# Optimization experiments

Measured on AMD Instinct MI355X. Metric: run time of the kernel, lower is better.

Reference implementation:

```python
import jax, jax.numpy as jnp
import numpy as np

B, N, D_IN = 8192, 32, 128   # batch, num_agents, obs_input_dim
D_PROC = 128                 # obs_output_dim
D_FIN = 128                  # final_input_dim
HID = 256                    # hard-coded policy hidden
A = 10                       # final_output_dim (num_actions)


def setup_inputs() -> dict:
    key = jax.random.key(0)
    ks = jax.random.split(key, 9)
    s = lambda k, shp: jax.random.normal(k, shp, dtype=jnp.float32) / jnp.sqrt(jnp.float32(shp[-1]))
    return {
        "states": jax.random.normal(ks[0], (B, N, D_IN), dtype=jnp.float32),
        "Wk1": s(ks[1], (D_PROC, D_IN)),
        "Wq1": s(ks[2], (D_PROC, D_IN)),
        "Wv1": s(ks[3], (D_PROC, D_IN)),
        "Wk2": s(ks[4], (D_FIN, D_PROC)),
        "Wq2": s(ks[5], (D_FIN, D_PROC)),
        "Wv2": s(ks[6], (D_FIN, D_PROC)),
        "Wp1": s(ks[7], (HID, D_FIN)),
        "Wp2": s(ks[8], (A, HID)),
    }


def reference(states, Wk1, Wq1, Wv1, Wk2, Wq2, Wv2, Wp1, Wp2):
    # NOTE: the original torch code scales BOTH attention blocks by
    # sqrt(self.d_k_obs) == sqrt(final_input_dim) (not d_k_obs_proc).
    inv_scale = 1.0 / jnp.sqrt(jnp.asarray(Wk2.shape[0], states.dtype))

    # ---- attention block 1 over agents ----
    k1 = jnp.einsum("bnd,ed->bne", states, Wk1)
    q1 = jnp.einsum("bnd,ed->bne", states, Wq1)
    v1 = jnp.einsum("bnd,ed->bne", states, Wv1)
    weight_1 = jax.nn.softmax(jnp.einsum("bne,bme->bnm", q1, k1) * inv_scale, axis=-1)
    wav = jnp.einsum("bnm,bme->bne", weight_1, v1)  # [B, N, D_PROC]

    # ---- attention block 2 ----
    k2 = jnp.einsum("bne,fe->bnf", wav, Wk2)
    q2 = jnp.einsum("bne,fe->bnf", wav, Wq2)
    v2 = jnp.einsum("bne,fe->bnf", wav, Wv2)
    weight = jax.nn.softmax(jnp.einsum("bnf,bmf->bnm", q2, k2) * inv_scale, axis=-1)
    node_features = jnp.einsum("bnm,bmf->bnf", weight, v2)  # [B, N, D_FIN]

    # ---- policy MLP head ----
    h = jax.nn.leaky_relu(jnp.einsum("bnf,hf->bnh", node_features, Wp1), negative_slope=0.01)
    policy = jax.nn.softmax(jnp.einsum("bnh,ah->bna", h, Wp2), axis=-1)
    return policy, weight_1, weight
```

## Files before the change

kernel.cpp:

```cpp
#include <hip/hip_runtime.h>
#include <stdint.h>

namespace {

typedef __attribute__((ext_vector_type(8)))  short short8;
typedef __attribute__((ext_vector_type(16))) float f32x16;
typedef __attribute__((ext_vector_type(4)))  float f32x4;

union U4 {
    uint4    q;
    uint32_t u[4];
    uint16_t us[8];
    short8   s8;
};

constexpr float INV_SCALE = 0.08838834764831845f;

constexpr size_t WSPROJ  = 32768;
constexpr size_t WP1OFF  = 4 * WSPROJ;
constexpr size_t WP2OFF  = WP1OFF + 65536;
constexpr size_t M1F_OFF = WP2OFF + 16384;
constexpr size_t M2F_OFF = M1F_OFF + 65536;

constexpr int AH_OFF = 0;
constexpr int TB_OFF = 16384;
constexpr int VT_OFF = 32768;
constexpr int S_OFF  = 49152;

__device__ __forceinline__ int pl_addr(int base, int n, int e) {
    return base + ((n * 256 + e * 2) ^ ((n & 15) << 4));
}
__device__ __forceinline__ int vt_addr(int e, int m) {
    return VT_OFF + ((e * 128 + m * 2) ^ ((e & 7) << 4));
}
__device__ __forceinline__ int s_addr(int n, int m) {
    return S_OFF + n * 144 + m * 4;
}
__device__ __forceinline__ int h_addr(int n, int h) {
    return TB_OFF + ((n * 512 + h * 2) ^ ((n & 15) << 4));
}
__device__ __forceinline__ int ps_addr(int n, int a) {
    return AH_OFF + n * 144 + a * 4;
}

__device__ __forceinline__ uint16_t f2bf_rne(float x) {
    uint32_t u = __float_as_uint(x);
    u += 0x7FFFu + ((u >> 16) & 1u);
    return (uint16_t)(u >> 16);
}

__device__ __forceinline__ uint32_t pack2_rne(float x0, float x1) {
    uint32_t u0 = __float_as_uint(x0); u0 += 0x7FFFu + ((u0 >> 16) & 1u);
    uint32_t u1 = __float_as_uint(x1); u1 += 0x7FFFu + ((u1 >> 16) & 1u);
    return __builtin_amdgcn_perm(u1, u0, 0x07060302u);
}

__device__ __forceinline__ void split8(float4 a, float4 b, short8& hi, short8& lo) {
    float xs[8] = {a.x, a.y, a.z, a.w, b.x, b.y, b.z, b.w};
    U4 h, l;
#pragma unroll
    for (int p = 0; p < 4; ++p) {
        uint32_t b0 = __float_as_uint(xs[2 * p]);
        uint32_t b1 = __float_as_uint(xs[2 * p + 1]);
        float r0 = xs[2 * p]     - __uint_as_float(b0 & 0xFFFF0000u);
        float r1 = xs[2 * p + 1] - __uint_as_float(b1 & 0xFFFF0000u);
        h.u[p] = __builtin_amdgcn_perm(b1, b0, 0x07060302u);
        l.u[p] = __builtin_amdgcn_perm(__float_as_uint(r1), __float_as_uint(r0), 0x07060302u);
    }
    hi = h.s8; lo = l.s8;
}

__device__ __forceinline__ void gemm_tv(const char* smem, const uint8_t* __restrict__ wb,
                                        int rowoff, int c, int l,
                                        f32x16& tacc, f32x16& vacc) {
    f32x16 z = {0.f,0.f,0.f,0.f, 0.f,0.f,0.f,0.f, 0.f,0.f,0.f,0.f, 0.f,0.f,0.f,0.f};
    tacc = z; vacc = z;
    const int n = rowoff + (l & 31), half = l >> 5;
#pragma unroll 1
    for (int kb = 0; kb < 8; ++kb) {
        const int d0 = kb * 16 + half * 8;
        U4 ah;
        ah.q = *(const uint4*)(smem + pl_addr(AH_OFF, n, d0));
        const uint8_t* p = wb + (size_t)(c * 8 + kb) * 1024 + (size_t)l * 16;
        U4 bm, bv;
        bm.q = *(const uint4*)p;
        tacc = __builtin_amdgcn_mfma_f32_32x32x16_bf16(ah.s8, bm.s8, tacc, 0, 0, 0);
        bv.q = *(const uint4*)(p + WSPROJ);
        vacc = __builtin_amdgcn_mfma_f32_32x32x16_bf16(ah.s8, bv.s8, vacc, 0, 0, 0);
    }
}

__device__ __forceinline__ void gemm_mlp2(const char* smem, const uint8_t* __restrict__ mb,
                                          int rowoff, int c, int l,
                                          f32x16& a0, f32x16& a1) {
    f32x16 z = {0.f,0.f,0.f,0.f, 0.f,0.f,0.f,0.f, 0.f,0.f,0.f,0.f, 0.f,0.f,0.f,0.f};
    a0 = z; a1 = z;
    const int n = rowoff + (l & 31), half = l >> 5;
#pragma unroll 1
    for (int kb = 0; kb < 8; ++kb) {
        const int d0 = kb * 16 + half * 8;
        U4 ah;
        ah.q = *(const uint4*)(smem + pl_addr(AH_OFF, n, d0));
        const uint8_t* p0 = mb + (size_t)((c)     * 8 + kb) * 1024 + (size_t)l * 16;
        const uint8_t* p1 = mb + (size_t)((c + 4) * 8 + kb) * 1024 + (size_t)l * 16;
        U4 b0, b1;
        b0.q = *(const uint4*)p0;
        a0 = __builtin_amdgcn_mfma_f32_32x32x16_bf16(ah.s8, b0.s8, a0, 0, 0, 0);
        b1.q = *(const uint4*)p1;
        a1 = __builtin_amdgcn_mfma_f32_32x32x16_bf16(ah.s8, b1.s8, a1, 0, 0, 0);
    }
}

__device__ __forceinline__ void store_plane32(char* smem, int base, int rowoff, int c, int l,
                                              const f32x16& a) {
    const int e = c * 32 + (l & 31);
    const int half = l >> 5;
#pragma unroll
    for (int r = 0; r < 16; ++r) {
        int n = rowoff + (r & 3) + 8 * (r >> 2) + 4 * half;
        *(uint16_t*)(smem + pl_addr(base, n, e)) = f2bf_rne(a[r]);
    }
}

__global__ void prep_m(const float* __restrict__ Wq1, const float* __restrict__ Wk1,
                       const float* __restrict__ Wq2, const float* __restrict__ Wk2,
                       uint8_t* __restrict__ wsb) {
    const int bid = blockIdx.x;
    const int mat = bid >> 7;
    const int dp  = bid & 127;
    const int d   = threadIdx.x;
    const float* Wq = mat ? Wq2 : Wq1;
    const float* Wk = mat ? Wk2 : Wk1;
    float s = 0.f;
#pragma unroll 4
    for (int e = 0; e < 128; ++e)
        s += Wq[e * 128 + d] * Wk[e * 128 + dp];
    float* mf = (float*)(wsb + (mat ? M2F_OFF : M1F_OFF));
    mf[dp * 128 + d] = s;
}

__global__ void prepack(const float* __restrict__ Wv1, const float* __restrict__ Wv2,
                        const float* __restrict__ Wp1, const float* __restrict__ Wp2,
                        uint8_t* __restrict__ wsb) {
    const int bid = blockIdx.x;
    const int l = threadIdx.x;
    float4 fa = make_float4(0.f, 0.f, 0.f, 0.f), fb = fa;
    uint8_t* dst;
    bool rne1 = true;
    if (bid < 128) {
        int m = bid >> 5, rem = bid & 31, c = rem >> 3, kb = rem & 7;
        const float* W = (m == 0) ? (const float*)(wsb + M1F_OFF)
                       : (m == 1) ? Wv1
                       : (m == 2) ? (const float*)(wsb + M2F_OFF)
                       : Wv2;
        int e  = c * 32 + (l & 31);
        int d0 = kb * 16 + (l >> 5) * 8;
        const float* src = W + e * 128 + d0;
        fa = *(const float4*)src;
        fb = *(const float4*)(src + 4);
        dst = wsb + (size_t)m * WSPROJ + (size_t)(c * 8 + kb) * 1024 + l * 16;
    } else if (bid < 192) {
        int idx = bid - 128, c = idx >> 3, kb = idx & 7;
        int e  = c * 32 + (l & 31);
        int d0 = kb * 16 + (l >> 5) * 8;
        const float* src = Wp1 + e * 128 + d0;
        fa = *(const float4*)src;
        fb = *(const float4*)(src + 4);
        dst = wsb + WP1OFF + (size_t)(c * 8 + kb) * 1024 + l * 16;
    } else {
        int kb = bid - 192;
        int a  = l & 15;
        int h0 = kb * 32 + ((l >> 4) & 3) * 8;
        if (a < 10) {
            const float* src = Wp2 + a * 256 + h0;
            fa = *(const float4*)src;
            fb = *(const float4*)(src + 4);
        }
        dst = wsb + WP2OFF + (size_t)(kb * 2) * 1024 + l * 16;
        rne1 = false;
    }
    if (rne1) {
        float xs[8] = {fa.x, fa.y, fa.z, fa.w, fb.x, fb.y, fb.z, fb.w};
        U4 hv;
#pragma unroll
        for (int i = 0; i < 8; ++i) hv.us[i] = f2bf_rne(xs[i]);
        *(short8*)dst = hv.s8;
    } else {
        short8 hi, lo;
        split8(fa, fb, hi, lo);
        *(short8*)dst = hi;
        *(short8*)(dst + 1024) = lo;
    }
}

__global__ __launch_bounds__(512, 4)
void fused_net(const float* __restrict__ states, const uint8_t* __restrict__ wsb,
               float* __restrict__ out_policy, float* __restrict__ out_w1,
               float* __restrict__ out_w2) {
    __shared__ __align__(16) char smem[58368];

    const int b2   = blockIdx.x;
    const int t    = threadIdx.x;
    const int w    = t >> 6;
    const int l    = t & 63;
    const int l31  = l & 31;
    const int half = l >> 5;
    const int l15  = l & 15;
    const int g4   = (l >> 4) & 3;
    const int rh   = w >> 2;
    const int c4   = w & 3;

    {
        const float* src = states + (size_t)b2 * 8192;
#pragma unroll
        for (int r = 0; r < 4; ++r) {
            int flat = (t + 512 * r) * 4;
            int n = flat >> 7, d0 = flat & 127;
            float4 v = *(const float4*)(src + flat);
            uint2 hw;
            hw.x = pack2_rne(v.x, v.y);
            hw.y = pack2_rne(v.z, v.w);
            *(uint2*)(smem + pl_addr(AH_OFF, n, d0)) = hw;
        }
    }
    __syncthreads();

#pragma unroll 1
    for (int blk = 0; blk < 2; ++blk) {
        const uint8_t* wb = wsb + (size_t)(blk * 2) * WSPROJ;

        {
            f32x16 tacc, vacc;
            gemm_tv(smem, wb, rh * 32, c4, l, tacc, vacc);
            store_plane32(smem, TB_OFF, rh * 32, c4, l, tacc);
            const int e = c4 * 32 + l31;
#pragma unroll
            for (int g = 0; g < 4; ++g) {
                int m0 = rh * 32 + 8 * g + 4 * half;
                uint2 pk;
                pk.x = pack2_rne(vacc[4 * g],     vacc[4 * g + 1]);
                pk.y = pack2_rne(vacc[4 * g + 2], vacc[4 * g + 3]);
                *(uint2*)(smem + vt_addr(e, m0)) = pk;
            }
        }
        __builtin_amdgcn_sched_barrier(0);
        __syncthreads();

        {
            const int bq = w >> 2, rb = (w >> 1) & 1, mb = w & 1;
            const int trow = bq * 32 + rb * 16 + l15;
            const int xrow = bq * 32 + mb * 16 + l15;
            f32x4 s4 = {0.f, 0.f, 0.f, 0.f};
#pragma unroll
            for (int kb = 0; kb < 4; ++kb) {
                int e0 = kb * 32 + g4 * 8;
                U4 th, xh;
                th.q = *(const uint4*)(smem + pl_addr(TB_OFF, trow, e0));
                xh.q = *(const uint4*)(smem + pl_addr(AH_OFF, xrow, e0));
                s4 = __builtin_amdgcn_mfma_f32_16x16x32_bf16(th.s8, xh.s8, s4, 0, 0, 0);
            }
#pragma unroll
            for (int r = 0; r < 4; ++r) {
                int n = bq * 32 + rb * 16 + g4 * 4 + r;
                *(float*)(smem + s_addr(n, mb * 16 + l15)) = s4[r] * INV_SCALE;
            }
        }
        __syncthreads();

        if (t < 128) {
            const int n = w * 32 + l31;
            float4 v0 = *(const float4*)(smem + s_addr(n, half * 16));
            float4 v1 = *(const float4*)(smem + s_addr(n, half * 16 + 4));
            float4 v2 = *(const float4*)(smem + s_addr(n, half * 16 + 8));
            float4 v3 = *(const float4*)(smem + s_addr(n, half * 16 + 12));
            float vv[16] = {v0.x, v0.y, v0.z, v0.w, v1.x, v1.y, v1.z, v1.w,
                            v2.x, v2.y, v2.z, v2.w, v3.x, v3.y, v3.z, v3.w};
            float mx = vv[0];
#pragma unroll
            for (int i = 1; i < 16; ++i) mx = fmaxf(mx, vv[i]);
            mx = fmaxf(mx, __shfl_xor(mx, 32));
            float sum = 0.f;
#pragma unroll
            for (int i = 0; i < 16; ++i) { vv[i] = __expf(vv[i] - mx); sum += vv[i]; }
            sum += __shfl_xor(sum, 32);
            float inv = 1.0f / sum;
#pragma unroll
            for (int i = 0; i < 16; ++i) vv[i] *= inv;
            *(float4*)(smem + s_addr(n, half * 16))      = make_float4(vv[0], vv[1], vv[2], vv[3]);
            *(float4*)(smem + s_addr(n, half * 16 + 4))  = make_float4(vv[4], vv[5], vv[6], vv[7]);
            *(float4*)(smem + s_addr(n, half * 16 + 8))  = make_float4(vv[8], vv[9], vv[10], vv[11]);
            *(float4*)(smem + s_addr(n, half * 16 + 12)) = make_float4(vv[12], vv[13], vv[14], vv[15]);
        }
        __syncthreads();

        {
            float* outw = blk ? out_w2 : out_w1;
            int f = t * 4;
            int n = f >> 5, m0 = f & 31;
            float4 o = *(const float4*)(smem + s_addr(n, m0));
            *(float4*)(outw + (size_t)b2 * 2048 + f) = o;
        }

        {
            const int bq = w >> 2;
            f32x16 pv = {0.f,0.f,0.f,0.f, 0.f,0.f,0.f,0.f, 0.f,0.f,0.f,0.f, 0.f,0.f,0.f,0.f};
            const int e = c4 * 32 + l31;
#pragma unroll
            for (int kb = 0; kb < 2; ++kb) {
                int m0 = kb * 16 + half * 8;
                float4 fa = *(const float4*)(smem + s_addr(bq * 32 + l31, m0));
                float4 fb = *(const float4*)(smem + s_addr(bq * 32 + l31, m0 + 4));
                short8 wh, wl;
                split8(fa, fb, wh, wl);
                U4 vh;
                vh.q = *(const uint4*)(smem + vt_addr(e, bq * 32 + m0));
                pv = __builtin_amdgcn_mfma_f32_32x32x16_bf16(wh, vh.s8, pv, 0, 0, 0);
                pv = __builtin_amdgcn_mfma_f32_32x32x16_bf16(wl, vh.s8, pv, 0, 0, 0);
            }
            store_plane32(smem, AH_OFF, bq * 32, c4, l, pv);
        }
        __builtin_amdgcn_sched_barrier(0);
        __syncthreads();
    }

    {
        f32x16 h0_, h1_;
        gemm_mlp2(smem, wsb + WP1OFF, rh * 32, c4, l, h0_, h1_);
#pragma unroll
        for (int rep = 0; rep < 2; ++rep) {
            const int hc = c4 + rep * 4;
            const int hcol = hc * 32 + l31;
#pragma unroll
            for (int r = 0; r < 16; ++r) {
                int n = rh * 32 + (r & 3) + 8 * (r >> 2) + 4 * half;
                float x = rep ? h1_[r] : h0_[r];
                x = fmaxf(x, 0.01f * x);
                *(uint16_t*)(smem + h_addr(n, hcol)) = f2bf_rne(x);
            }
        }
    }
    __syncthreads();

    if (w < 4) {
        f32x4 acc = {0.f, 0.f, 0.f, 0.f};
        const int n = w * 16 + l15;
#pragma unroll
        for (int kb = 0; kb < 8; ++kb) {
            int h0 = kb * 32 + g4 * 8;
            U4 a;
            a.q = *(const uint4*)(smem + h_addr(n, h0));
            const uint8_t* p = wsb + WP2OFF + (size_t)(kb * 2) * 1024 + (size_t)l * 16;
            U4 bh, bl;
            bh.q = *(const uint4*)p;
            bl.q = *(const uint4*)(p + 1024);
            acc = __builtin_amdgcn_mfma_f32_16x16x32_bf16(a.s8, bh.s8, acc, 0, 0, 0);
            acc = __builtin_amdgcn_mfma_f32_16x16x32_bf16(a.s8, bl.s8, acc, 0, 0, 0);
        }
#pragma unroll
        for (int r = 0; r < 4; ++r) {
            int nn = w * 16 + g4 * 4 + r;
            *(float*)(smem + ps_addr(nn, l15)) = acc[r];
        }
    }
    __syncthreads();

    if (t < 64) {
        float v[10];
#pragma unroll
        for (int a2 = 0; a2 < 10; ++a2) v[a2] = *(const float*)(smem + ps_addr(t, a2));
        float mx = v[0];
#pragma unroll
        for (int a2 = 1; a2 < 10; ++a2) mx = fmaxf(mx, v[a2]);
        float sum = 0.f;
#pragma unroll
        for (int a2 = 0; a2 < 10; ++a2) { v[a2] = __expf(v[a2] - mx); sum += v[a2]; }
        float inv = 1.0f / sum;
#pragma unroll
        for (int a2 = 0; a2 < 10; ++a2) *(float*)(smem + ps_addr(t, a2)) = v[a2] * inv;
    }
    __syncthreads();

    for (int o = t; o < 640; o += 512) {
        int n = o / 10, a2 = o - n * 10;
        out_policy[(size_t)b2 * 640 + o] = *(const float*)(smem + ps_addr(n, a2));
    }
}

}

extern "C" void kernel_launch(void* const* d_in, const int* in_sizes, int n_in,
                              void* d_out, int out_size, void* d_ws, size_t ws_size,
                              hipStream_t stream) {
    const float* states = (const float*)d_in[0];
    const float* Wk1 = (const float*)d_in[1];
    const float* Wq1 = (const float*)d_in[2];
    const float* Wv1 = (const float*)d_in[3];
    const float* Wk2 = (const float*)d_in[4];
    const float* Wq2 = (const float*)d_in[5];
    const float* Wv2 = (const float*)d_in[6];
    const float* Wp1 = (const float*)d_in[7];
    const float* Wp2 = (const float*)d_in[8];

    const int B = in_sizes[0] / 4096;

    uint8_t* wsb = (uint8_t*)d_ws;
    float* out        = (float*)d_out;
    float* out_policy = out;
    float* out_w1     = out_policy + (size_t)B * 320;
    float* out_w2     = out_w1 + (size_t)B * 1024;

    hipLaunchKernelGGL(prep_m, dim3(256), dim3(128), 0, stream,
                       Wq1, Wk1, Wq2, Wk2, wsb);
    hipLaunchKernelGGL(prepack, dim3(200), dim3(64), 0, stream,
                       Wv1, Wv2, Wp1, Wp2, wsb);
    hipLaunchKernelGGL(fused_net, dim3(B / 2), dim3(512), 0, stream,
                       states, wsb, out_policy, out_w1, out_w2);
}
```

Baseline: 138.3 us.

## Parallelize softmax across all threads, fuse output store, use single bf16 P plane

```diff
diff --git a/kernel.cpp b/kernel.cpp
--- a/kernel.cpp
+++ b/kernel.cpp
@@ -26,6 +26,7 @@
 constexpr int TB_OFF = 16384;
 constexpr int VT_OFF = 32768;
 constexpr int S_OFF  = 49152;
+constexpr int P_OFF  = 58368;
 
 __device__ __forceinline__ int pl_addr(int base, int n, int e) {
     return base + ((n * 256 + e * 2) ^ ((n & 15) << 4));
@@ -35,6 +36,9 @@
 }
 __device__ __forceinline__ int s_addr(int n, int m) {
     return S_OFF + n * 144 + m * 4;
+}
+__device__ __forceinline__ int p_addr(int n, int m) {
+    return P_OFF + n * 72 + m * 2;
 }
 __device__ __forceinline__ int h_addr(int n, int h) {
     return TB_OFF + ((n * 512 + h * 2) ^ ((n & 15) << 4));
@@ -136,7 +140,7 @@
     for (int e = 0; e < 128; ++e)
         s += Wq[e * 128 + d] * Wk[e * 128 + dp];
     float* mf = (float*)(wsb + (mat ? M2F_OFF : M1F_OFF));
-    mf[dp * 128 + d] = s;
+    mf[dp * 128 + d] = s * INV_SCALE;
 }
 
 __global__ void prepack(const float* __restrict__ Wv1, const float* __restrict__ Wv2,
@@ -197,7 +201,7 @@
 void fused_net(const float* __restrict__ states, const uint8_t* __restrict__ wsb,
                float* __restrict__ out_policy, float* __restrict__ out_w1,
                float* __restrict__ out_w2) {
-    __shared__ __align__(16) char smem[58368];
+    __shared__ __align__(16) char smem[62976];
 
     const int b2   = blockIdx.x;
     const int t    = threadIdx.x;
@@ -262,44 +266,35 @@
 #pragma unroll
             for (int r = 0; r < 4; ++r) {
                 int n = bq * 32 + rb * 16 + g4 * 4 + r;
-                *(float*)(smem + s_addr(n, mb * 16 + l15)) = s4[r] * INV_SCALE;
+                *(float*)(smem + s_addr(n, mb * 16 + l15)) = s4[r];
             }
         }
         __syncthreads();
 
-        if (t < 128) {
-            const int n = w * 32 + l31;
-            float4 v0 = *(const float4*)(smem + s_addr(n, half * 16));
-            float4 v1 = *(const float4*)(smem + s_addr(n, half * 16 + 4));
-            float4 v2 = *(const float4*)(smem + s_addr(n, half * 16 + 8));
-            float4 v3 = *(const float4*)(smem + s_addr(n, half * 16 + 12));
-            float vv[16] = {v0.x, v0.y, v0.z, v0.w, v1.x, v1.y, v1.z, v1.w,
-                            v2.x, v2.y, v2.z, v2.w, v3.x, v3.y, v3.z, v3.w};
-            float mx = vv[0];
-#pragma unroll
-            for (int i = 1; i < 16; ++i) mx = fmaxf(mx, vv[i]);
-            mx = fmaxf(mx, __shfl_xor(mx, 32));
-            float sum = 0.f;
-#pragma unroll
-            for (int i = 0; i < 16; ++i) { vv[i] = __expf(vv[i] - mx); sum += vv[i]; }
-            sum += __shfl_xor(sum, 32);
-            float inv = 1.0f / sum;
-#pragma unroll
-            for (int i = 0; i < 16; ++i) vv[i] *= inv;
-            *(float4*)(smem + s_addr(n, half * 16))      = make_float4(vv[0], vv[1], vv[2], vv[3]);
-            *(float4*)(smem + s_addr(n, half * 16 + 4))  = make_float4(vv[4], vv[5], vv[6], vv[7]);
-            *(float4*)(smem + s_addr(n, half * 16 + 8))  = make_float4(vv[8], vv[9], vv[10], vv[11]);
-            *(float4*)(smem + s_addr(n, half * 16 + 12)) = make_float4(vv[12], vv[13], vv[14], vv[15]);
+        {
+            const int n  = t >> 3;
+            const int mq = (t & 7) * 4;
+            float4 v = *(const float4*)(smem + s_addr(n, mq));
+            float mx = fmaxf(fmaxf(v.x, v.y), fmaxf(v.z, v.w));
+            mx = fmaxf(mx, __shfl_xor(mx, 1));
+            mx = fmaxf(mx, __shfl_xor(mx, 2));
+            mx = fmaxf(mx, __shfl_xor(mx, 4));
+            v.x = __expf(v.x - mx); v.y = __expf(v.y - mx);
+            v.z = __expf(v.z - mx); v.w = __expf(v.w - mx);
+            float s = v.x + v.y + v.z + v.w;
+            s += __shfl_xor(s, 1);
+            s += __shfl_xor(s, 2);
+            s += __shfl_xor(s, 4);
+            float inv = 1.0f / s;
+            v.x *= inv; v.y *= inv; v.z *= inv; v.w *= inv;
+            float* outw = blk ? out_w2 : out_w1;
+            *(float4*)(outw + (size_t)b2 * 2048 + n * 32 + mq) = v;
+            uint2 pb;
+            pb.x = pack2_rne(v.x, v.y);
+            pb.y = pack2_rne(v.z, v.w);
+            *(uint2*)(smem + p_addr(n, mq)) = pb;
         }
         __syncthreads();
-
-        {
-            float* outw = blk ? out_w2 : out_w1;
-            int f = t * 4;
-            int n = f >> 5, m0 = f & 31;
-            float4 o = *(const float4*)(smem + s_addr(n, m0));
-            *(float4*)(outw + (size_t)b2 * 2048 + f) = o;
-        }
 
         {
             const int bq = w >> 2;
@@ -308,14 +303,12 @@
 #pragma unroll
             for (int kb = 0; kb < 2; ++kb) {
                 int m0 = kb * 16 + half * 8;
-                float4 fa = *(const float4*)(smem + s_addr(bq * 32 + l31, m0));
-                float4 fb = *(const float4*)(smem + s_addr(bq * 32 + l31, m0 + 4));
-                short8 wh, wl;
-                split8(fa, fb, wh, wl);
-                U4 vh;
+                U4 pa, vh;
+                int pbase = p_addr(bq * 32 + l31, m0);
+                *(uint2*)&pa.u[0] = *(const uint2*)(smem + pbase);
+                *(uint2*)&pa.u[2] = *(const uint2*)(smem + pbase + 8);
                 vh.q = *(const uint4*)(smem + vt_addr(e, bq * 32 + m0));
-                pv = __builtin_amdgcn_mfma_f32_32x32x16_bf16(wh, vh.s8, pv, 0, 0, 0);
-                pv = __builtin_amdgcn_mfma_f32_32x32x16_bf16(wl, vh.s8, pv, 0, 0, 0);
+                pv = __builtin_amdgcn_mfma_f32_32x32x16_bf16(pa.s8, vh.s8, pv, 0, 0, 0);
             }
             store_plane32(smem, AH_OFF, bq * 32, c4, l, pv);
         }
```

Result: no change. 136.4 us (-1.4%).
